# Optimization experiments

Measured on AMD Instinct MI355X. Metric: run time of the kernel, lower is better.

## Reference

```python
import jax, jax.numpy as jnp
import numpy as np

EPS = 1e-5


def setup_inputs() -> dict:
    key = jax.random.key(0)
    ks = jax.random.split(key, 24)
    B, S, D = 32, 1024, 768        # batch, num_segs, feature_dim
    E, G, C, P = 2, 8, 64, 384     # expansion, groups, num_clusters, latent_clus_dim
    EF = E * D                     # 1536
    GFS = EF // G                  # group_feature_size = 192
    s = 0.02
    f32 = jnp.float32
    return {
        "x": jax.random.normal(ks[0], (B, S, D), f32),
        "W_exp": s * jax.random.normal(ks[1], (D, EF), f32),
        "b_exp": jnp.zeros((EF,), f32),
        "W_ga": s * jax.random.normal(ks[2], (EF, G), f32),
        "b_ga": jnp.zeros((G,), f32),
        "bn1_g": jnp.ones((G * C,), f32) + 0.1 * jax.random.normal(ks[3], (G * C,), f32),
        "bn1_b": 0.1 * jax.random.normal(ks[4], (G * C,), f32),
        "bn1_m": 0.05 * jax.random.normal(ks[5], (G * C,), f32),
        "bn1_v": 1.0 + 0.1 * jax.random.uniform(ks[6], (G * C,), f32),
        "cluster_weights": s * jax.random.normal(ks[7], (EF, G * C), f32),
        "W_proj": s * jax.random.normal(ks[8], (GFS, D), f32),
        "b_proj": jnp.zeros((D,), f32),
        "bn2_g": jnp.ones((C,), f32) + 0.1 * jax.random.normal(ks[9], (C,), f32),
        "bn2_b": 0.1 * jax.random.normal(ks[10], (C,), f32),
        "bn2_m": 0.05 * jax.random.normal(ks[11], (C,), f32),
        "bn2_v": 1.0 + 0.1 * jax.random.uniform(ks[12], (C,), f32),
        "Wq": s * jax.random.normal(ks[13], (D, P), f32),
        "bq": jnp.zeros((P,), f32),
        "Wkv": s * jax.random.normal(ks[14], (D, 2 * P), f32),
        "bkv": jnp.zeros((2 * P,), f32),
        "Wp2": s * jax.random.normal(ks[15], (P, D), f32),
        "bp2": jnp.zeros((D,), f32),
    }


def reference(x, W_exp, b_exp, W_ga, b_ga, bn1_g, bn1_b, bn1_m, bn1_v,
              cluster_weights, W_proj, b_proj, bn2_g, bn2_b, bn2_m, bn2_v,
              Wq, bq, Wkv, bkv, Wp2, bp2):
    B, S, D = x.shape
    EF = W_exp.shape[1]
    G = W_ga.shape[1]
    C = bn2_g.shape[0]
    GFS = EF // G
    P = Wq.shape[1]

    fea = x @ W_exp + b_exp                                   # (B,S,EF)
    ga = jax.nn.sigmoid(fea @ W_ga + b_ga).reshape(B, S * G)  # (B,S*G)

    act = fea.reshape(B * S, EF) @ cluster_weights            # (B*S, G*C)
    act = (act - bn1_m) * (bn1_g / jnp.sqrt(bn1_v + EPS)) + bn1_b  # eval BN
    act = jax.nn.softmax(act.reshape(B, S * G, C), axis=-1) * ga[:, :, None]

    fea_g = fea.reshape(B, S * G, GFS)
    cent = jnp.einsum('bnc,bnf->bcf', act, fea_g)             # (B,C,GFS)

    nc = cent @ W_proj + b_proj                               # (B,C,D)
    scale2 = (bn2_g / jnp.sqrt(bn2_v + EPS))[None, :, None]
    nc = (nc - bn2_m[None, :, None]) * scale2 + bn2_b[None, :, None]

    q = x @ Wq + bq                                           # (B,S,P)
    kv = (nc @ Wkv + bkv).reshape(B, C, 2, P)
    k, v = kv[:, :, 0], kv[:, :, 1]

    scores = jnp.einsum('bsp,bcp->bsc', q, k) / jnp.sqrt(jnp.float32(P))
    attn = jax.nn.softmax(scores, axis=-1)                    # (B,S,C)
    out = jnp.einsum('bsc,bcp->bsp', attn, v)                 # (B,S,P)
    return out @ Wp2 + bp2                                    # (B,S,D)
```

## Files before the change

### kernel.cpp

```cpp
#include <hip/hip_runtime.h>
#include <hip/hip_bf16.h>

#define EPSV 1e-5f

namespace {
constexpr int Bn = 32, Sn = 1024, Dn = 768, Gn = 8, Cn = 64, Pn = 384;
constexpr int EFn = 1536, GFSn = 192, Nrows = Bn * Sn;
}

typedef __attribute__((ext_vector_type(8))) short short8;
typedef __attribute__((ext_vector_type(4))) float f32x4;
typedef __attribute__((ext_vector_type(16))) float f32x16;

__device__ __forceinline__ ushort f2bf(float f) {
  uint u = __builtin_bit_cast(uint, f);
  uint r = (u + 0x7fffu + ((u >> 16) & 1u)) >> 16;
  return (ushort)r;
}
__device__ __forceinline__ uint pack2bf(float lo, float hi) {
  return (uint)f2bf(lo) | ((uint)f2bf(hi) << 16);
}
__device__ __forceinline__ float bf2f(ushort h) {
  return __builtin_bit_cast(float, (uint)h << 16);
}
__device__ __forceinline__ void load16(const ushort* g, ushort* l) {
  __builtin_amdgcn_global_load_lds(
      (const __attribute__((address_space(1))) void*)g,
      (__attribute__((address_space(3))) void*)l, 16, 0, 0);
}
__device__ __forceinline__ int xcd_lid() {
  const int nbx = gridDim.x;
  const int nwg = nbx * gridDim.y;
  const int orig = blockIdx.y * nbx + blockIdx.x;
  const int xq = nwg >> 3, xr = nwg & 7;
  const int xcd = orig & 7, xi = orig >> 3;
  return (xcd < xr ? xcd * (xq + 1) : xr * (xq + 1) + (xcd - xr) * xq) + xi;
}

template <int MODE>
__global__ __launch_bounds__(256) void gemm_bf16(
    const ushort* __restrict__ A, const ushort* __restrict__ BT,
    const float* __restrict__ bias, void* __restrict__ Cout,
    int M, int N, int K,
    const float* __restrict__ g2, const float* __restrict__ b2,
    const float* __restrict__ m2, const float* __restrict__ v2,
    const float* __restrict__ bias2, ushort* __restrict__ kq,
    ushort* __restrict__ vt) {
  __shared__ ushort sh[24576];
  const int tid = threadIdx.x;
  const int wave = tid >> 6, lane = tid & 63;
  const int nbx = gridDim.x;
  const int lid = xcd_lid();
  const int gm = (lid / nbx) * 128, gn = (lid % nbx) * 128;
  const int wr = wave >> 1, wc = wave & 1;

  const int sws = ((tid & 3) ^ ((tid >> 3) & 3)) * 8;
  const int c0 = tid, c1 = tid + 256;
  const ushort* gA0 = A + (size_t)(gm + (c0 >> 2)) * K + sws;
  const ushort* gA1 = A + (size_t)(gm + (c1 >> 2)) * K + sws;
  const ushort* gB0 = BT + (size_t)(gn + (c0 >> 2)) * K + sws;
  const ushort* gB1 = BT + (size_t)(gn + (c1 >> 2)) * K + sws;

  f32x4 acc[4][4] = {};
  const int l15 = lane & 15;
  const int arow = wr * 64 + l15;
  const int brow = wc * 64 + l15;
  const int kswz = (((lane >> 4) ^ ((l15 >> 1) & 3))) * 8;
  const int nk = K >> 5;

#define GB_STAGE(buf, k0)                                    \
  {                                                          \
    load16(gA0 + (k0), &sh[(buf)*8192 + wave * 512]);        \
    load16(gA1 + (k0), &sh[(buf)*8192 + 2048 + wave * 512]); \
    load16(gB0 + (k0), &sh[(buf)*8192 + 4096 + wave * 512]); \
    load16(gB1 + (k0), &sh[(buf)*8192 + 6144 + wave * 512]); \
  }

  GB_STAGE(0, 0);
  GB_STAGE(1, 32);
  int bc = 0;
  for (int t = 0; t < nk; ++t) {
    if (t + 1 < nk) {
      asm volatile("s_waitcnt vmcnt(4)" ::: "memory");
    } else {
      asm volatile("s_waitcnt vmcnt(0)" ::: "memory");
    }
    __builtin_amdgcn_s_barrier();
    __builtin_amdgcn_sched_barrier(0);
    if (t + 2 < nk) {
      const int bp = (bc == 0) ? 2 : bc - 1;
      GB_STAGE(bp, (t + 2) * 32);
    }
    short8 a[4], b[4];
#pragma unroll
    for (int m = 0; m < 4; ++m)
      a[m] = *reinterpret_cast<const short8*>(
          &sh[bc * 8192 + (arow + m * 16) * 32 + kswz]);
#pragma unroll
    for (int n = 0; n < 4; ++n)
      b[n] = *reinterpret_cast<const short8*>(
          &sh[bc * 8192 + 4096 + (brow + n * 16) * 32 + kswz]);
    __builtin_amdgcn_s_setprio(1);
#pragma unroll
    for (int m = 0; m < 4; ++m)
#pragma unroll
      for (int n = 0; n < 4; ++n)
        acc[m][n] = __builtin_amdgcn_mfma_f32_16x16x32_bf16(
            a[m], b[n], acc[m][n], 0, 0, 0);
    __builtin_amdgcn_s_setprio(0);
    __builtin_amdgcn_sched_barrier(0);
    bc = (bc == 2) ? 0 : bc + 1;
  }
#undef GB_STAGE

  const int crow0 = gm + wr * 64 + (lane >> 4) * 4;
  const int ccol0 = gn + wc * 64 + l15;
  float sc_[4][4], sf_[4][4];
  if (MODE == 2) {
#pragma unroll
    for (int m = 0; m < 4; ++m)
#pragma unroll
      for (int j = 0; j < 4; ++j) {
        const int c = (crow0 + m * 16 + j) & 63;
        const float s = g2[c] * rsqrtf(v2[c] + EPSV);
        sc_[m][j] = s;
        sf_[m][j] = b2[c] - m2[c] * s;
      }
  }
#pragma unroll
  for (int m = 0; m < 4; ++m)
#pragma unroll
    for (int n = 0; n < 4; ++n) {
      const int col = ccol0 + n * 16;
      const float bv = (MODE == 4)
                           ? (col < 1536 ? bias[col] : bias2[col - 1536])
                           : (bias ? bias[col] : 0.f);
#pragma unroll
      for (int j = 0; j < 4; ++j) {
        const int row = crow0 + m * 16 + j;
        float v = acc[m][n][j] + bv;
        if (MODE == 2) {
          v = v * sc_[m][j] + sf_[m][j];
          ((ushort*)Cout)[(size_t)row * N + col] = f2bf(v);
        } else if (MODE == 3) {
          const ushort h = f2bf(v);
          if (col < 384) {
            kq[(size_t)row * 384 + col] = h;
          } else {
            vt[(size_t)(row >> 6) * 24576 + (size_t)(col - 384) * 64 +
               (row & 63)] = h;
          }
        } else if (MODE == 4) {
          const ushort h = f2bf(v);
          if (gn < 1536)
            ((ushort*)Cout)[(size_t)row * 1536 + col] = h;
          else
            kq[(size_t)row * 384 + (col - 1536)] = h;
        }
      }
    }
}

__global__ __launch_bounds__(256) void gemm_breg(
    const ushort* __restrict__ A, const ushort* __restrict__ BT,
    const float* __restrict__ bias, float* __restrict__ Cout,
    int M, int N, int K) {
  __shared__ ushort sh[12288];
  const int tid = threadIdx.x;
  const int wave = tid >> 6, lane = tid & 63;
  const int nbx = gridDim.x;
  const int lid = xcd_lid();
  const int gm = (lid / nbx) * 128, gn = (lid % nbx) * 128;
  const int wr = wave >> 1, wc = wave & 1;

  const int sws = ((tid & 3) ^ ((tid >> 3) & 3)) * 8;
  const int c0 = tid, c1 = tid + 256;
  const ushort* gA0 = A + (size_t)(gm + (c0 >> 2)) * K + sws;
  const ushort* gA1 = A + (size_t)(gm + (c1 >> 2)) * K + sws;

  f32x4 acc[4][4] = {};
  const int l15 = lane & 15;
  const int arow = wr * 64 + l15;
  const int koff = (lane >> 4) * 8;
  const ushort* gBr = BT + (size_t)(gn + wc * 64 + l15) * K + koff;
  const int kswz = (((lane >> 4) ^ ((l15 >> 1) & 3))) * 8;
  const int nk = K >> 5;
  int bc = 0;

#define BR_STAGE(buf, k0)                                    \
  {                                                          \
    load16(gA0 + (k0), &sh[(buf)*4096 + wave * 512]);        \
    load16(gA1 + (k0), &sh[(buf)*4096 + 2048 + wave * 512]); \
  }
#define BR_LOADB(dst, k0)                                          \
  {                                                                \
    _Pragma("unroll") for (int n = 0; n < 4; ++n) dst[n] =         \
        *reinterpret_cast<const uint4*>(gBr + (size_t)(n * 16) * K \
                                        + (k0));                   \
  }
#define BR_ITER(u, bcur, bnxt)                                        \
  {                                                                   \
    if ((u) + 1 < nk)                                                 \
      asm volatile("s_waitcnt vmcnt(2)" ::: "memory");                \
    else                                                              \
      asm volatile("s_waitcnt vmcnt(0)" ::: "memory");                \
    __builtin_amdgcn_s_barrier();                                     \
    __builtin_amdgcn_sched_barrier(0);                                \
    if ((u) + 1 < nk) BR_LOADB(bnxt, ((u) + 1) * 32);                 \
    __builtin_amdgcn_sched_barrier(0);                                \
    if ((u) + 2 < nk) {                                               \
      const int bp = (bc == 0) ? 2 : bc - 1;                          \
      BR_STAGE(bp, ((u) + 2) * 32);                                   \
    }                                                                 \
    __builtin_amdgcn_sched_barrier(0);                                \
    short8 a[4];                                                      \
    _Pragma("unroll") for (int m = 0; m < 4; ++m) a[m] =              \
        *reinterpret_cast<const short8*>(                             \
            &sh[bc * 4096 + (arow + m * 16) * 32 + kswz]);            \
    __builtin_amdgcn_s_setprio(1);                                    \
    _Pragma("unroll") for (int m = 0; m < 4; ++m)                     \
        _Pragma("unroll") for (int n = 0; n < 4; ++n) acc[m][n] =     \
            __builtin_amdgcn_mfma_f32_16x16x32_bf16(                  \
                a[m], __builtin_bit_cast(short8, bcur[n]), acc[m][n], \
                0, 0, 0);                                             \
    __builtin_amdgcn_s_setprio(0);                                    \
    __builtin_amdgcn_sched_barrier(0);                                \
    bc = (bc == 2) ? 0 : bc + 1;                                      \
  }

  uint4 b0[4], b1[4];
  BR_STAGE(0, 0);
  __builtin_amdgcn_sched_barrier(0);
  BR_LOADB(b0, 0);
  __builtin_amdgcn_sched_barrier(0);
  BR_STAGE(1, 32);
  for (int t = 0; t < nk; t += 2) {
    BR_ITER(t, b0, b1);
    BR_ITER(t + 1, b1, b0);
  }
#undef BR_ITER
#undef BR_LOADB
#undef BR_STAGE

  const int crow0 = gm + wr * 64 + (lane >> 4) * 4;
  const int ccol0 = gn + wc * 64 + l15;
#pragma unroll
  for (int m = 0; m < 4; ++m)
#pragma unroll
    for (int n = 0; n < 4; ++n) {
      const int col = ccol0 + n * 16;
      const float bv = bias ? bias[col] : 0.f;
#pragma unroll
      for (int j = 0; j < 4; ++j)
        Cout[(size_t)(crow0 + m * 16 + j) * N + col] = acc[m][n][j] + bv;
    }
}

__global__ __launch_bounds__(256) void gemm_ga(
    const ushort* __restrict__ fea, const ushort* __restrict__ WTga,
    const float* __restrict__ b_ga, float* __restrict__ ga) {
  constexpr int K = EFn;
  __shared__ ushort sh[13824];
  const int tid = threadIdx.x;
  const int wave = tid >> 6, lane = tid & 63;
  const int gm = blockIdx.x * 128;

  const int sws = ((tid & 3) ^ ((tid >> 3) & 3)) * 8;
  const int swsB = ((lane & 3) ^ ((lane >> 3) & 3)) * 8;
  const int c0 = tid, c1 = tid + 256;
  const ushort* gA0 = fea + (size_t)(gm + (c0 >> 2)) * K + sws;
  const ushort* gA1 = fea + (size_t)(gm + (c1 >> 2)) * K + sws;
  const ushort* gB = WTga + (size_t)(lane >> 2) * K + swsB;

  f32x4 acc[2] = {};
  const int l15 = lane & 15, l4 = lane >> 4;
  const int kswz = ((l4 ^ ((l15 >> 1) & 3))) * 8;
  constexpr int nk = K / 32;

#define GA_STAGE(buf, k0)                                     \
  {                                                           \
    load16(gA0 + (k0), &sh[(buf)*4608 + wave * 512]);         \
    load16(gA1 + (k0), &sh[(buf)*4608 + 2048 + wave * 512]);  \
    if (wave == 0) load16(gB + (k0), &sh[(buf)*4608 + 4096]); \
  }

  GA_STAGE(0, 0);
  GA_STAGE(1, 32);
  int bc = 0;
  for (int t = 0; t < nk; ++t) {
    if (t + 1 < nk) {
      if (wave == 0)
        asm volatile("s_waitcnt vmcnt(3)" ::: "memory");
      else
        asm volatile("s_waitcnt vmcnt(2)" ::: "memory");
    } else {
      asm volatile("s_waitcnt vmcnt(0)" ::: "memory");
    }
    __builtin_amdgcn_s_barrier();
    __builtin_amdgcn_sched_barrier(0);
    if (t + 2 < nk) {
      const int bp = (bc == 0) ? 2 : bc - 1;
      GA_STAGE(bp, (t + 2) * 32);
    }
    const short8 b = *reinterpret_cast<const short8*>(
        &sh[bc * 4608 + 4096 + l15 * 32 + kswz]);
    short8 a[2];
#pragma unroll
    for (int mi = 0; mi < 2; ++mi)
      a[mi] = *reinterpret_cast<const short8*>(
          &sh[bc * 4608 + (wave * 32 + mi * 16 + l15) * 32 + kswz]);
    __builtin_amdgcn_s_setprio(1);
#pragma unroll
    for (int mi = 0; mi < 2; ++mi)
      acc[mi] =
          __builtin_amdgcn_mfma_f32_16x16x32_bf16(a[mi], b, acc[mi], 0, 0, 0);
    __builtin_amdgcn_s_setprio(0);
    __builtin_amdgcn_sched_barrier(0);
    bc = (bc == 2) ? 0 : bc + 1;
  }
#undef GA_STAGE

  if (l15 < 8) {
    const float bv = b_ga[l15];
#pragma unroll
    for (int mi = 0; mi < 2; ++mi)
#pragma unroll
      for (int j = 0; j < 4; ++j) {
        const int row = gm + wave * 32 + mi * 16 + l4 * 4 + j;
        const float v = acc[mi][j] + bv;
        ga[(size_t)row * 8 + l15] = 1.0f / (1.0f + expf(-v));
      }
  }
}

__global__ __launch_bounds__(256) void gemm_sm(
    const ushort* __restrict__ A, const ushort* __restrict__ BT,
    const float* __restrict__ g1, const float* __restrict__ b1,
    const float* __restrict__ m1, const float* __restrict__ v1,
    const float* __restrict__ ga, ushort* __restrict__ actT) {
  constexpr int K = EFn, N = Nrows;
  __shared__ ushort sh[24576];
  __shared__ float sScale[128], sShift[128];
  const int tid = threadIdx.x;
  const int wave = tid >> 6, lane = tid & 63;
  const int lid = xcd_lid();
  const int gm = (lid & 3) * 128;
  const int gn = (lid >> 2) * 128;
  const int wr = wave >> 1, wc = wave & 1;

  if (tid < 128) {
    const int row = gm + tid;
    const float sc = g1[row] * rsqrtf(v1[row] + EPSV);
    sScale[tid] = sc;
    sShift[tid] = b1[row] - m1[row] * sc;
  }

  const int sws = ((tid & 3) ^ ((tid >> 3) & 3)) * 8;
  const int c0 = tid, c1 = tid + 256;
  const ushort* gA0 = A + (size_t)(gm + (c0 >> 2)) * K + sws;
  const ushort* gA1 = A + (size_t)(gm + (c1 >> 2)) * K + sws;
  const ushort* gB0 = BT + (size_t)(gn + (c0 >> 2)) * K + sws;
  const ushort* gB1 = BT + (size_t)(gn + (c1 >> 2)) * K + sws;

  f32x4 acc[4][4] = {};
  const int l15 = lane & 15;
  const int arow = wr * 64 + l15;
  const int brow = wc * 64 + l15;
  const int kswz = (((lane >> 4) ^ ((l15 >> 1) & 3))) * 8;
  constexpr int nk = K >> 5;

#define SM_STAGE(buf, k0)                                    \
  {                                                          \
    load16(gA0 + (k0), &sh[(buf)*8192 + wave * 512]);        \
    load16(gA1 + (k0), &sh[(buf)*8192 + 2048 + wave * 512]); \
    load16(gB0 + (k0), &sh[(buf)*8192 + 4096 + wave * 512]); \
    load16(gB1 + (k0), &sh[(buf)*8192 + 6144 + wave * 512]); \
  }

  SM_STAGE(0, 0);
  SM_STAGE(1, 32);
  int bc = 0;
  for (int t = 0; t < nk; ++t) {
    if (t + 1 < nk) {
      asm volatile("s_waitcnt vmcnt(4)" ::: "memory");
    } else {
      asm volatile("s_waitcnt vmcnt(0)" ::: "memory");
    }
    __builtin_amdgcn_s_barrier();
    __builtin_amdgcn_sched_barrier(0);
    if (t + 2 < nk) {
      const int bp = (bc == 0) ? 2 : bc - 1;
      SM_STAGE(bp, (t + 2) * 32);
    }
    short8 a[4], b[4];
#pragma unroll
    for (int m = 0; m < 4; ++m)
      a[m] = *reinterpret_cast<const short8*>(
          &sh[bc * 8192 + (arow + m * 16) * 32 + kswz]);
#pragma unroll
    for (int n = 0; n < 4; ++n)
      b[n] = *reinterpret_cast<const short8*>(
          &sh[bc * 8192 + 4096 + (brow + n * 16) * 32 + kswz]);
    __builtin_amdgcn_s_setprio(1);
#pragma unroll
    for (int m = 0; m < 4; ++m)
#pragma unroll
      for (int n = 0; n < 4; ++n)
        acc[m][n] = __builtin_amdgcn_mfma_f32_16x16x32_bf16(
            a[m], b[n], acc[m][n], 0, 0, 0);
    __builtin_amdgcn_s_setprio(0);
    __builtin_amdgcn_sched_barrier(0);
    bc = (bc == 2) ? 0 : bc + 1;
  }
#undef SM_STAGE

  const int l4 = lane >> 4;
  const int g = (gm >> 6) + wr;
#pragma unroll
  for (int n = 0; n < 4; ++n) {
    const int col = gn + wc * 64 + n * 16 + l15;
    float mx = -1e30f;
#pragma unroll
    for (int m = 0; m < 4; ++m)
#pragma unroll
      for (int j = 0; j < 4; ++j) {
        const int rl = wr * 64 + m * 16 + l4 * 4 + j;
        acc[m][n][j] = acc[m][n][j] * sScale[rl] + sShift[rl];
        mx = fmaxf(mx, acc[m][n][j]);
      }
    mx = fmaxf(mx, __shfl_xor(mx, 16));
    mx = fmaxf(mx, __shfl_xor(mx, 32));
    float sum = 0.f;
#pragma unroll
    for (int m = 0; m < 4; ++m)
#pragma unroll
      for (int j = 0; j < 4; ++j) {
        acc[m][n][j] = expf(acc[m][n][j] - mx);
        sum += acc[m][n][j];
      }
    sum += __shfl_xor(sum, 16);
    sum += __shfl_xor(sum, 32);
    const float sc = ga[(size_t)col * 8 + g] / sum;
#pragma unroll
    for (int m = 0; m < 4; ++m)
#pragma unroll
      for (int j = 0; j < 4; ++j) {
        const int rowg = gm + wr * 64 + m * 16 + l4 * 4 + j;
        actT[(size_t)rowg * N + col] = f2bf(acc[m][n][j] * sc);
      }
  }
}

__global__ __launch_bounds__(256) void cvt_kernel(const float* __restrict__ in,
                                                  ushort* __restrict__ out,
                                                  int n4) {
  const int i = blockIdx.x * 256 + threadIdx.x;
  if (i >= n4) return;
  const float4 v = reinterpret_cast<const float4*>(in)[i];
  ushort4 o;
  o.x = f2bf(v.x); o.y = f2bf(v.y); o.z = f2bf(v.z); o.w = f2bf(v.w);
  reinterpret_cast<ushort4*>(out)[i] = o;
}

__global__ __launch_bounds__(256) void tconv_kernel(const float* __restrict__ in,
                                                    ushort* __restrict__ out,
                                                    int R, int C) {
  __shared__ float t[32][33];
  const int tx = threadIdx.x & 31, ty = threadIdx.x >> 5;
  const int bc = blockIdx.x * 32, br = blockIdx.y * 32;
#pragma unroll
  for (int i = 0; i < 32; i += 8)
    t[ty + i][tx] = in[(size_t)(br + ty + i) * C + bc + tx];
  __syncthreads();
#pragma unroll
  for (int i = 0; i < 32; i += 8)
    out[(size_t)(bc + ty + i) * R + br + tx] = f2bf(t[tx][ty + i]);
}

__global__ __launch_bounds__(256) void gawt_kernel(const float* __restrict__ in,
                                                   ushort* __restrict__ out) {
  const int k = blockIdx.x * 256 + threadIdx.x;
#pragma unroll
  for (int g = 0; g < 8; ++g) {
    out[(size_t)g * EFn + k] = f2bf(in[(size_t)k * 8 + g]);
    out[(size_t)(g + 8) * EFn + k] = 0;
  }
}

__global__ __launch_bounds__(256) void cent_mfma(
    const ushort* __restrict__ actT, const ushort* __restrict__ fea,
    float* __restrict__ part) {
  __shared__ ushort As[2][64 * 64];
  __shared__ ushort Bs[2][192 * 64];
  const int tid = threadIdx.x;
  const int wave = tid >> 6, lane = tid & 63;
  const int b = blockIdx.x >> 4;
  const int g = (blockIdx.x >> 1) & 7;
  const int ch = blockIdx.x & 1;
  const size_t colbase = (size_t)b * 1024 + ch * 512;
  const int srow = tid >> 2, scp = (tid & 3) * 2;
  const ushort* gA = actT + (size_t)(g * 64 + srow) * Nrows + colbase;
  const int bseg = tid % 24;
  const int bsg = tid / 24;
  const bool bact = tid < 192;
  const ushort* gB =
      fea + (size_t)(colbase + bsg * 8) * EFn + g * 192 + bseg * 8;

  uint4 ra[2], rbv[8];
  f32x4 acc[4][3] = {};
  const int l15 = lane & 15, hi = lane >> 4;
  const int sw = srow & 7;

#define CM_ISSUE(k0)                                                        \
  {                                                                         \
    _Pragma("unroll") for (int i = 0; i < 2; ++i) ra[i] =                   \
        *reinterpret_cast<const uint4*>(gA + (k0) + (scp + i) * 8);         \
    if (bact) {                                                             \
      _Pragma("unroll") for (int i = 0; i < 8; ++i) rbv[i] =                \
          *reinterpret_cast<const uint4*>(gB + (size_t)((k0) + i) * EFn);   \
    }                                                                       \
  }
#define CM_STASH(buf)                                                       \
  {                                                                         \
    _Pragma("unroll") for (int i = 0; i < 2; ++i) {                         \
      const int c = scp + i;                                                \
      *reinterpret_cast<uint4*>(&As[buf][srow * 64 + ((c ^ sw) * 8)]) =     \
          ra[i];                                                            \
    }                                                                       \
    if (bact) {                                                             \
      const ushort* rin = reinterpret_cast<const ushort*>(rbv);             \
      _Pragma("unroll") for (int e = 0; e < 8; ++e) {                       \
        alignas(16) ushort tmp[8];                                          \
        _Pragma("unroll") for (int i = 0; i < 8; ++i) tmp[i] =              \
            rin[i * 8 + e];                                                 \
        const int r = bseg * 8 + e;                                         \
        *reinterpret_cast<uint4*>(&Bs[buf][r * 64 + ((bsg ^ (r & 7)) * 8)]) \
            = *reinterpret_cast<const uint4*>(tmp);                         \
      }                                                                     \
    }                                                                       \
  }

  CM_ISSUE(0);
  CM_STASH(0);
  for (int kk = 0; kk < 8; ++kk) {
    const int buf = kk & 1;
    __syncthreads();
    if (kk < 7) CM_ISSUE((kk + 1) * 64);
#pragma unroll
    for (int ks = 0; ks < 2; ++ks) {
      const int chh = ks * 4 + hi;
      short8 a[4], bb[3];
#pragma unroll
      for (int m = 0; m < 4; ++m) {
        const int r = m * 16 + l15;
        a[m] = *reinterpret_cast<const short8*>(
            &As[buf][r * 64 + ((chh ^ (r & 7)) * 8)]);
      }
#pragma unroll
      for (int nn = 0; nn < 3; ++nn) {
        const int r = wave * 48 + nn * 16 + l15;
        bb[nn] = *reinterpret_cast<const short8*>(
            &Bs[buf][r * 64 + ((chh ^ (r & 7)) * 8)]);
      }
#pragma unroll
      for (int m = 0; m < 4; ++m)
#pragma unroll
        for (int nn = 0; nn < 3; ++nn)
          acc[m][nn] = __builtin_amdgcn_mfma_f32_16x16x32_bf16(
              a[m], bb[nn], acc[m][nn], 0, 0, 0);
    }
    if (kk < 7) CM_STASH(buf ^ 1);
  }
#undef CM_ISSUE
#undef CM_STASH

  float* pb = part + (size_t)blockIdx.x * 12288;
#pragma unroll
  for (int m = 0; m < 4; ++m)
#pragma unroll
    for (int nn = 0; nn < 3; ++nn) {
      const int col = wave * 48 + nn * 16 + l15;
#pragma unroll
      for (int j = 0; j < 4; ++j) {
        const int row = m * 16 + hi * 4 + j;
        pb[row * 192 + col] = acc[m][nn][j];
      }
    }
}

__global__ __launch_bounds__(256) void cent_reduce8(
    const float* __restrict__ part, ushort* __restrict__ cent) {
  const int idx = blockIdx.x * 256 + threadIdx.x;
  const int b = idx / 12288, r = idx % 12288;
  float s = 0.f;
#pragma unroll
  for (int j = 0; j < 16; ++j) s += part[(size_t)(b * 16 + j) * 12288 + r];
  cent[idx] = f2bf(s);
}

__global__ __launch_bounds__(256) void attn_mfma(
    const ushort* __restrict__ qb, const ushort* __restrict__ kb,
    const ushort* __restrict__ vtb, ushort* __restrict__ aout) {
  const int wave = threadIdx.x >> 6, lane = threadIdx.x & 63;
  const int wrow = blockIdx.x * 4 + wave;
  const int row0 = wrow * 32;
  const int b = row0 >> 10;
  const int l31 = lane & 31, hi = lane >> 5;

  f32x16 accs0 = 0.f, accs1 = 0.f;
  const ushort* qp = qb + (size_t)(row0 + l31) * 384 + hi * 8;
  const ushort* kp = kb + (size_t)(b * 64 + l31) * 384 + hi * 8;
#pragma unroll 4
  for (int ks = 0; ks < 24; ++ks) {
    const short8 bq = *reinterpret_cast<const short8*>(qp + ks * 16);
    const short8 a0 = *reinterpret_cast<const short8*>(kp + ks * 16);
    const short8 a1 = *reinterpret_cast<const short8*>(kp + 32 * 384 + ks * 16);
    accs0 = __builtin_amdgcn_mfma_f32_32x32x16_bf16(a0, bq, accs0, 0, 0, 0);
    accs1 = __builtin_amdgcn_mfma_f32_32x32x16_bf16(a1, bq, accs1, 0, 0, 0);
  }

  const float alpha = 0.05103103630798287f;
  float p[32];
#pragma unroll
  for (int i = 0; i < 16; ++i) { p[i] = accs0[i]; p[16 + i] = accs1[i]; }
  float mx = p[0];
#pragma unroll
  for (int i = 1; i < 32; ++i) mx = fmaxf(mx, p[i]);
  mx = fmaxf(mx, __shfl_xor(mx, 32));
  float sum = 0.f;
#pragma unroll
  for (int i = 0; i < 32; ++i) {
    p[i] = expf((p[i] - mx) * alpha);
    sum += p[i];
  }
  sum += __shfl_xor(sum, 32);
  const float inv = 1.0f / sum;

  uint pk0[8], pk1[8];
#pragma unroll
  for (int ct = 0; ct < 2; ++ct)
#pragma unroll
    for (int rg = 0; rg < 4; ++rg) {
      pk0[ct * 4 + rg] =
          pack2bf(p[ct * 16 + rg * 4 + 0] * inv, p[ct * 16 + rg * 4 + 1] * inv);
      pk1[ct * 4 + rg] =
          pack2bf(p[ct * 16 + rg * 4 + 2] * inv, p[ct * 16 + rg * 4 + 3] * inv);
    }
  uint ex0[8], ex1[8];
#pragma unroll
  for (int i = 0; i < 8; ++i) {
    ex0[i] = __shfl_xor(pk0[i], 32);
    ex1[i] = __shfl_xor(pk1[i], 32);
  }

  const ushort* vp = vtb + ((size_t)b * 384 + l31) * 64 + hi * 8;
  ushort* orow = aout + (size_t)(row0 + l31) * 384;
  for (int mt = 0; mt < 12; ++mt) {
    f32x16 acco = 0.f;
#pragma unroll
    for (int kc = 0; kc < 4; ++kc) {
      const short8 av = *reinterpret_cast<const short8*>(
          vp + (size_t)mt * 32 * 64 + kc * 16);
      const int base = (kc >> 1) * 4 + (kc & 1) * 2;
      const uint o0 = hi ? pk0[base + 1] : pk0[base];
      const uint o1 = hi ? pk1[base + 1] : pk1[base];
      const uint e0 = hi ? ex0[base + 1] : ex0[base];
      const uint e1 = hi ? ex1[base + 1] : ex1[base];
      uint4 uu;
      uu.x = hi ? e0 : o0;
      uu.y = hi ? e1 : o1;
      uu.z = hi ? o0 : e0;
      uu.w = hi ? o1 : e1;
      const short8 bp = __builtin_bit_cast(short8, uu);
      acco = __builtin_amdgcn_mfma_f32_32x32x16_bf16(av, bp, acco, 0, 0, 0);
    }
#pragma unroll
    for (int rg = 0; rg < 4; ++rg) {
      ushort4 ov;
      ov.x = f2bf(acco[rg * 4 + 0]);
      ov.y = f2bf(acco[rg * 4 + 1]);
      ov.z = f2bf(acco[rg * 4 + 2]);
      ov.w = f2bf(acco[rg * 4 + 3]);
      *reinterpret_cast<ushort4*>(&orow[mt * 32 + rg * 8 + hi * 4]) = ov;
    }
  }
}

extern "C" void kernel_launch(void* const* d_in, const int* in_sizes, int n_in,
                              void* d_out, int out_size, void* d_ws,
                              size_t ws_size, hipStream_t stream) {
  (void)in_sizes; (void)n_in; (void)out_size; (void)ws_size;
  const float* x      = (const float*)d_in[0];
  const float* W_exp  = (const float*)d_in[1];
  const float* b_exp  = (const float*)d_in[2];
  const float* W_ga   = (const float*)d_in[3];
  const float* b_ga   = (const float*)d_in[4];
  const float* bn1_g  = (const float*)d_in[5];
  const float* bn1_b  = (const float*)d_in[6];
  const float* bn1_m  = (const float*)d_in[7];
  const float* bn1_v  = (const float*)d_in[8];
  const float* cw     = (const float*)d_in[9];
  const float* W_proj = (const float*)d_in[10];
  const float* b_proj = (const float*)d_in[11];
  const float* bn2_g  = (const float*)d_in[12];
  const float* bn2_b  = (const float*)d_in[13];
  const float* bn2_m  = (const float*)d_in[14];
  const float* bn2_v  = (const float*)d_in[15];
  const float* Wq     = (const float*)d_in[16];
  const float* bq     = (const float*)d_in[17];
  const float* Wkv    = (const float*)d_in[18];
  const float* bkv    = (const float*)d_in[19];
  const float* Wp2    = (const float*)d_in[20];
  const float* bp2    = (const float*)d_in[21];
  float* out = (float*)d_out;

  char* ws = (char*)d_ws;
  ushort* fea   = (ushort*)(ws + 0);
  ushort* aout  = (ushort*)(ws + 0);
  ushort* xb    = (ushort*)(ws + 100663296ull);
  ushort* actT  = (ushort*)(ws + 100663296ull);
  ushort* q_bf  = (ushort*)(ws + 150994944ull);
  float*  ga    = (float*)(ws + 176160768ull);
  float*  part  = (float*)(ws + 177209344ull);
  ushort* WTcat = (ushort*)(ws + 202375168ull);
  ushort* WT2   = (ushort*)(ws + 205324288ull);
  ushort* WT4   = (ushort*)(ws + 206897152ull);
  ushort* WT5   = (ushort*)(ws + 207486976ull);
  ushort* WT6   = (ushort*)(ws + 207781888ull);
  ushort* WTga  = (ushort*)(ws + 208961536ull);
  ushort* cent  = (ushort*)(ws + 209010688ull);
  ushort* nc    = (ushort*)(ws + 209797120ull);
  ushort* k_bf  = (ushort*)(ws + 212942848ull);
  ushort* vT_bf = (ushort*)(ws + 214515712ull);

  dim3 blk(256);
  cvt_kernel<<<dim3((Nrows * Dn / 4 + 255) / 256), blk, 0, stream>>>(
      x, xb, Nrows * Dn / 4);
  tconv_kernel<<<dim3(EFn / 32, Dn / 32), blk, 0, stream>>>(W_exp, WTcat, Dn,
                                                            EFn);
  tconv_kernel<<<dim3(Pn / 32, Dn / 32), blk, 0, stream>>>(
      Wq, WTcat + (size_t)1536 * 768, Dn, Pn);
  tconv_kernel<<<dim3(512 / 32, EFn / 32), blk, 0, stream>>>(cw, WT2, EFn, 512);
  tconv_kernel<<<dim3(Dn / 32, Pn / 32), blk, 0, stream>>>(Wp2, WT4, Pn, Dn);
  tconv_kernel<<<dim3(Dn / 32, GFSn / 32), blk, 0, stream>>>(W_proj, WT5, GFSn,
                                                             Dn);
  tconv_kernel<<<dim3(Dn / 32, Dn / 32), blk, 0, stream>>>(Wkv, WT6, Dn, Dn);
  gawt_kernel<<<dim3(EFn / 256), blk, 0, stream>>>(W_ga, WTga);
  gemm_bf16<4><<<dim3(1920 / 128, Nrows / 128), blk, 0, stream>>>(
      xb, WTcat, b_exp, fea, Nrows, 1920, Dn,
      nullptr, nullptr, nullptr, nullptr, bq, q_bf, nullptr);
  gemm_ga<<<dim3(Nrows / 128), blk, 0, stream>>>(fea, WTga, b_ga, ga);
  gemm_sm<<<dim3(Nrows / 128, 512 / 128), blk, 0, stream>>>(
      WT2, fea, bn1_g, bn1_b, bn1_m, bn1_v, ga, actT);
  cent_mfma<<<dim3(Bn * Gn * 2), blk, 0, stream>>>(actT, fea, part);
  cent_reduce8<<<dim3(393216 / 256), blk, 0, stream>>>(part, cent);
  gemm_bf16<2><<<dim3(Dn / 128, 2048 / 128), blk, 0, stream>>>(
      cent, WT5, b_proj, nc, 2048, Dn, GFSn,
      bn2_g, bn2_b, bn2_m, bn2_v, nullptr, nullptr, nullptr);
  gemm_bf16<3><<<dim3(Dn / 128, 2048 / 128), blk, 0, stream>>>(
      nc, WT6, bkv, nullptr, 2048, Dn, Dn,
      nullptr, nullptr, nullptr, nullptr, nullptr, k_bf, vT_bf);
  attn_mfma<<<dim3(Nrows / 128), blk, 0, stream>>>(q_bf, k_bf, vT_bf, aout);
  gemm_breg<<<dim3(Dn / 128, Nrows / 128), blk, 0, stream>>>(
      aout, WT4, bp2, out, Nrows, Dn, Pn);
}
```

Measured before the change: 413.4 us.

## Use deeper B-register prefetch GEMM for the expansion GEMM; swap the final projection to LDS GEMM

The B-from-registers GEMM is rewritten with three B register buffers, so B loads are issued three k-steps ahead and after the MFMAs, with tuned vmcnt waits. The large fused x@[W_exp|Wq] GEMM now uses this kernel instead of the LDS-staged gemm_bf16. The final out@Wp2 GEMM moves to gemm_bf16 (new MODE 0). This is meant to hide global-load latency in the biggest GEMM, at the cost of more registers and hand-counted waitcnt values that must stay correct.

```diff
diff --git a/kernel.cpp b/kernel.cpp
--- a/kernel.cpp
+++ b/kernel.cpp
@@ -44,8 +44,7 @@
     int M, int N, int K,
     const float* __restrict__ g2, const float* __restrict__ b2,
     const float* __restrict__ m2, const float* __restrict__ v2,
-    const float* __restrict__ bias2, ushort* __restrict__ kq,
-    ushort* __restrict__ vt) {
+    ushort* __restrict__ kq, ushort* __restrict__ vt) {
   __shared__ ushort sh[24576];
   const int tid = threadIdx.x;
   const int wave = tid >> 6, lane = tid & 63;
@@ -132,14 +131,16 @@
 #pragma unroll
     for (int n = 0; n < 4; ++n) {
       const int col = ccol0 + n * 16;
-      const float bv = (MODE == 4)
-                           ? (col < 1536 ? bias[col] : bias2[col - 1536])
-                           : (bias ? bias[col] : 0.f);
+      const float bv = bias ? bias[col] : 0.f;
 #pragma unroll
       for (int j = 0; j < 4; ++j) {
         const int row = crow0 + m * 16 + j;
         float v = acc[m][n][j] + bv;
-        if (MODE == 2) {
+        if (MODE == 0) {
+          ((float*)Cout)[(size_t)row * N + col] = v;
+        } else if (MODE == 1) {
+          ((ushort*)Cout)[(size_t)row * N + col] = f2bf(v);
+        } else if (MODE == 2) {
           v = v * sc_[m][j] + sf_[m][j];
           ((ushort*)Cout)[(size_t)row * N + col] = f2bf(v);
         } else if (MODE == 3) {
@@ -150,21 +151,17 @@
             vt[(size_t)(row >> 6) * 24576 + (size_t)(col - 384) * 64 +
                (row & 63)] = h;
           }
-        } else if (MODE == 4) {
-          const ushort h = f2bf(v);
-          if (gn < 1536)
-            ((ushort*)Cout)[(size_t)row * 1536 + col] = h;
-          else
-            kq[(size_t)row * 384 + (col - 1536)] = h;
         }
       }
     }
 }
 
-__global__ __launch_bounds__(256) void gemm_breg(
+template <int MODE>
+__global__ __launch_bounds__(256) void gemm_breg2(
     const ushort* __restrict__ A, const ushort* __restrict__ BT,
-    const float* __restrict__ bias, float* __restrict__ Cout,
-    int M, int N, int K) {
+    const float* __restrict__ bias, void* __restrict__ Cout,
+    int M, int N, int K,
+    const float* __restrict__ bias2, ushort* __restrict__ kq) {
   __shared__ ushort sh[12288];
   const int tid = threadIdx.x;
   const int wave = tid >> 6, lane = tid & 63;
@@ -174,9 +171,8 @@
   const int wr = wave >> 1, wc = wave & 1;
 
   const int sws = ((tid & 3) ^ ((tid >> 3) & 3)) * 8;
-  const int c0 = tid, c1 = tid + 256;
-  const ushort* gA0 = A + (size_t)(gm + (c0 >> 2)) * K + sws;
-  const ushort* gA1 = A + (size_t)(gm + (c1 >> 2)) * K + sws;
+  const ushort* gA0 = A + (size_t)(gm + (tid >> 2)) * K + sws;
+  const ushort* gA1 = A + (size_t)(gm + 64 + (tid >> 2)) * K + sws;
 
   f32x4 acc[4][4] = {};
   const int l15 = lane & 15;
@@ -185,62 +181,66 @@
   const ushort* gBr = BT + (size_t)(gn + wc * 64 + l15) * K + koff;
   const int kswz = (((lane >> 4) ^ ((l15 >> 1) & 3))) * 8;
   const int nk = K >> 5;
-  int bc = 0;
-
-#define BR_STAGE(buf, k0)                                    \
+
+  uint4 b0[4], b1[4], b2[4];
+
+#define BR2_STAGE(buf, k0)                                   \
   {                                                          \
     load16(gA0 + (k0), &sh[(buf)*4096 + wave * 512]);        \
     load16(gA1 + (k0), &sh[(buf)*4096 + 2048 + wave * 512]); \
   }
-#define BR_LOADB(dst, k0)                                          \
+#define BR2_LOADB(dst, k0)                                         \
   {                                                                \
     _Pragma("unroll") for (int n = 0; n < 4; ++n) dst[n] =         \
         *reinterpret_cast<const uint4*>(gBr + (size_t)(n * 16) * K \
                                         + (k0));                   \
   }
-#define BR_ITER(u, bcur, bnxt)                                        \
-  {                                                                   \
-    if ((u) + 1 < nk)                                                 \
-      asm volatile("s_waitcnt vmcnt(2)" ::: "memory");                \
-    else                                                              \
-      asm volatile("s_waitcnt vmcnt(0)" ::: "memory");                \
-    __builtin_amdgcn_s_barrier();                                     \
-    __builtin_amdgcn_sched_barrier(0);                                \
-    if ((u) + 1 < nk) BR_LOADB(bnxt, ((u) + 1) * 32);                 \
-    __builtin_amdgcn_sched_barrier(0);                                \
-    if ((u) + 2 < nk) {                                               \
-      const int bp = (bc == 0) ? 2 : bc - 1;                          \
-      BR_STAGE(bp, ((u) + 2) * 32);                                   \
-    }                                                                 \
-    __builtin_amdgcn_sched_barrier(0);                                \
-    short8 a[4];                                                      \
-    _Pragma("unroll") for (int m = 0; m < 4; ++m) a[m] =              \
-        *reinterpret_cast<const short8*>(                             \
-            &sh[bc * 4096 + (arow + m * 16) * 32 + kswz]);            \
-    __builtin_amdgcn_s_setprio(1);                                    \
-    _Pragma("unroll") for (int m = 0; m < 4; ++m)                     \
-        _Pragma("unroll") for (int n = 0; n < 4; ++n) acc[m][n] =     \
-            __builtin_amdgcn_mfma_f32_16x16x32_bf16(                  \
-                a[m], __builtin_bit_cast(short8, bcur[n]), acc[m][n], \
-                0, 0, 0);                                             \
-    __builtin_amdgcn_s_setprio(0);                                    \
-    __builtin_amdgcn_sched_barrier(0);                                \
-    bc = (bc == 2) ? 0 : bc + 1;                                      \
-  }
-
-  uint4 b0[4], b1[4];
-  BR_STAGE(0, 0);
+#define BR2_ITER(u, BB, BC)                                              \
+  {                                                                      \
+    if ((u) == 0)                                                        \
+      asm volatile("s_waitcnt vmcnt(2)" ::: "memory");                   \
+    else if ((u) == 1)                                                   \
+      asm volatile("s_waitcnt vmcnt(6)" ::: "memory");                   \
+    else if ((u) + 2 < nk)                                               \
+      asm volatile("s_waitcnt vmcnt(10)" ::: "memory");                  \
+    else if ((u) + 1 < nk)                                               \
+      asm volatile("s_waitcnt vmcnt(6)" ::: "memory");                   \
+    else                                                                 \
+      asm volatile("s_waitcnt vmcnt(0)" ::: "memory");                   \
+    __builtin_amdgcn_s_barrier();                                        \
+    __builtin_amdgcn_sched_barrier(0);                                   \
+    if ((u) + 2 < nk) BR2_STAGE(((BC) + 2) % 3, ((u) + 2) * 32);         \
+    short8 a[4];                                                         \
+    _Pragma("unroll") for (int m = 0; m < 4; ++m) a[m] =                 \
+        *reinterpret_cast<const short8*>(                                \
+            &sh[(BC)*4096 + (arow + m * 16) * 32 + kswz]);               \
+    __builtin_amdgcn_s_setprio(1);                                       \
+    _Pragma("unroll") for (int m = 0; m < 4; ++m)                        \
+        _Pragma("unroll") for (int n = 0; n < 4; ++n) acc[m][n] =        \
+            __builtin_amdgcn_mfma_f32_16x16x32_bf16(                     \
+                a[m], __builtin_bit_cast(short8, BB[n]), acc[m][n], 0,   \
+                0, 0);                                                   \
+    __builtin_amdgcn_s_setprio(0);                                       \
+    if ((u) + 3 < nk) BR2_LOADB(BB, ((u) + 3) * 32);                     \
+    __builtin_amdgcn_sched_barrier(0);                                   \
+  }
+
+  BR2_LOADB(b0, 0);
+  BR2_LOADB(b1, 32);
+  BR2_LOADB(b2, 64);
   __builtin_amdgcn_sched_barrier(0);
-  BR_LOADB(b0, 0);
+  BR2_STAGE(0, 0);
   __builtin_amdgcn_sched_barrier(0);
-  BR_STAGE(1, 32);
-  for (int t = 0; t < nk; t += 2) {
-    BR_ITER(t, b0, b1);
-    BR_ITER(t + 1, b1, b0);
-  }
-#undef BR_ITER
-#undef BR_LOADB
-#undef BR_STAGE
+  BR2_STAGE(1, 32);
+  __builtin_amdgcn_sched_barrier(0);
+  for (int t = 0; t < nk; t += 3) {
+    BR2_ITER(t, b0, 0);
+    BR2_ITER(t + 1, b1, 1);
+    BR2_ITER(t + 2, b2, 2);
+  }
+#undef BR2_ITER
+#undef BR2_LOADB
+#undef BR2_STAGE
 
   const int crow0 = gm + wr * 64 + (lane >> 4) * 4;
   const int ccol0 = gn + wc * 64 + l15;
@@ -249,10 +249,23 @@
 #pragma unroll
     for (int n = 0; n < 4; ++n) {
       const int col = ccol0 + n * 16;
-      const float bv = bias ? bias[col] : 0.f;
-#pragma unroll
-      for (int j = 0; j < 4; ++j)
-        Cout[(size_t)(crow0 + m * 16 + j) * N + col] = acc[m][n][j] + bv;
+      const float bv = (MODE == 4)
+                           ? (col < 1536 ? bias[col] : bias2[col - 1536])
+                           : (bias ? bias[col] : 0.f);
+#pragma unroll
+      for (int j = 0; j < 4; ++j) {
+        const int row = crow0 + m * 16 + j;
+        const float v = acc[m][n][j] + bv;
+        if (MODE == 4) {
+          const ushort h = f2bf(v);
+          if (gn < 1536)
+            ((ushort*)Cout)[(size_t)row * 1536 + col] = h;
+          else
+            kq[(size_t)row * 384 + (col - 1536)] = h;
+        } else {
+          ((float*)Cout)[(size_t)row * N + col] = v;
+        }
+      }
     }
 }
 
@@ -746,9 +759,8 @@
                                                              Dn);
   tconv_kernel<<<dim3(Dn / 32, Dn / 32), blk, 0, stream>>>(Wkv, WT6, Dn, Dn);
   gawt_kernel<<<dim3(EFn / 256), blk, 0, stream>>>(W_ga, WTga);
-  gemm_bf16<4><<<dim3(1920 / 128, Nrows / 128), blk, 0, stream>>>(
-      xb, WTcat, b_exp, fea, Nrows, 1920, Dn,
-      nullptr, nullptr, nullptr, nullptr, bq, q_bf, nullptr);
+  gemm_breg2<4><<<dim3(1920 / 128, Nrows / 128), blk, 0, stream>>>(
+      xb, WTcat, b_exp, fea, Nrows, 1920, Dn, bq, q_bf);
   gemm_ga<<<dim3(Nrows / 128), blk, 0, stream>>>(fea, WTga, b_ga, ga);
   gemm_sm<<<dim3(Nrows / 128, 512 / 128), blk, 0, stream>>>(
       WT2, fea, bn1_g, bn1_b, bn1_m, bn1_v, ga, actT);
@@ -756,11 +768,12 @@
   cent_reduce8<<<dim3(393216 / 256), blk, 0, stream>>>(part, cent);
   gemm_bf16<2><<<dim3(Dn / 128, 2048 / 128), blk, 0, stream>>>(
       cent, WT5, b_proj, nc, 2048, Dn, GFSn,
-      bn2_g, bn2_b, bn2_m, bn2_v, nullptr, nullptr, nullptr);
+      bn2_g, bn2_b, bn2_m, bn2_v, nullptr, nullptr);
   gemm_bf16<3><<<dim3(Dn / 128, 2048 / 128), blk, 0, stream>>>(
       nc, WT6, bkv, nullptr, 2048, Dn, Dn,
-      nullptr, nullptr, nullptr, nullptr, nullptr, k_bf, vT_bf);
+      nullptr, nullptr, nullptr, nullptr, k_bf, vT_bf);
   attn_mfma<<<dim3(Nrows / 128), blk, 0, stream>>>(q_bf, k_bf, vT_bf, aout);
-  gemm_breg<<<dim3(Dn / 128, Nrows / 128), blk, 0, stream>>>(
-      aout, WT4, bp2, out, Nrows, Dn, Pn);
-}
+  gemm_bf16<0><<<dim3(Dn / 128, Nrows / 128), blk, 0, stream>>>(
+      aout, WT4, bp2, out, Nrows, Dn, Pn,
+      nullptr, nullptr, nullptr, nullptr, nullptr, nullptr);
+}
```

After: 481.3 us. 1.16x slower.
